# Performance work log

Measured on AMD Instinct MI355X. Metric: run time of the kernel, lower is better.

The kernel has to match this reference:

```python
import jax, jax.numpy as jnp
import numpy as np

B, N, D_U = 32, 4096, 64
D = 128          # mlp_dim == model dim after MLP
H = 2            # n_heads
DH = D // H


def setup_inputs() -> dict:
    key = jax.random.key(0)
    ks = jax.random.split(key, 16)
    sc = lambda fan_in: 1.0 / np.sqrt(fan_in)
    inp = {
        "u": jax.random.normal(ks[0], (B, N, D_U), dtype=jnp.float32),
        "x": jax.random.uniform(ks[1], (B, N, 2), dtype=jnp.float32),
        # MLP params: [D_U -> D -> D], gelu after each hidden layer
        "W1": jax.random.normal(ks[2], (D_U, D), dtype=jnp.float32) * sc(D_U),
        "b1": jnp.zeros((D,), jnp.float32),
        "W2": jax.random.normal(ks[3], (D, D), dtype=jnp.float32) * sc(D),
        "b2": jnp.zeros((D,), jnp.float32),
        # learned pooling query (nn.Embed(1, D))
        "embed": jax.random.normal(ks[4], (1, D), dtype=jnp.float32),
        # multihead linear attention projections
        "Wq": jax.random.normal(ks[5], (D, D), dtype=jnp.float32) * sc(D),
        "bq": jnp.zeros((D,), jnp.float32),
        "Wk": jax.random.normal(ks[6], (D, D), dtype=jnp.float32) * sc(D),
        "bk": jnp.zeros((D,), jnp.float32),
        "Wv": jax.random.normal(ks[7], (D, D), dtype=jnp.float32) * sc(D),
        "bv": jnp.zeros((D,), jnp.float32),
        "Wo": jax.random.normal(ks[8], (D, D), dtype=jnp.float32) * sc(D),
        "bo": jnp.zeros((D,), jnp.float32),
    }
    return inp


def reference(u, x, W1, b1, W2, b2, embed, Wq, bq, Wk, bk, Wv, bv, Wo, bo):
    # MLP on set elements: [B, N, D_U] -> [B, N, D]
    z = jax.nn.gelu(u @ W1 + b1)
    z = jax.nn.gelu(z @ W2 + b2)

    n = z.shape[1]
    # learned query broadcast over batch: [B, 1, D]
    s = jnp.broadcast_to(embed[None, :, :], (z.shape[0], 1, z.shape[-1]))

    # multihead linear (Galerkin-style, softmax-free) attention
    q = (s @ Wq + bq).reshape(z.shape[0], 1, H, DH)   # [B, 1, H, DH]
    k = (z @ Wk + bk).reshape(z.shape[0], n, H, DH)   # [B, N, H, DH]
    v = (z @ Wv + bv).reshape(z.shape[0], n, H, DH)   # [B, N, H, DH]

    # context = K^T V / N per head: [B, H, DH, DH]
    context = jnp.einsum("bnhd,bnhe->bhde", k, v) / n
    out = jnp.einsum("bqhd,bhde->bqhe", q, context)   # [B, 1, H, DH]
    out = out.reshape(z.shape[0], 1, D) @ Wo + bo     # [B, 1, D]

    return out[:, 0, :]                               # [B, D]
```

## Files before the change

### kernel.cpp

```cpp
#include <hip/hip_runtime.h>
#include <math.h>

#define Bsz 32
#define Nn  4096
#define DU  64
#define Dm  128

#define GRID_MLP 512
#define BPB 16

#define WS_WKQ 0
#define WS_BKQ 256
#define WS_CNT 288
#define WS_A   320
#define WS_S   384
#define WS_WP  8576

#define H1STR 136

typedef short frag_ab __attribute__((ext_vector_type(8)));
typedef float frag_cd __attribute__((ext_vector_type(4)));

__device__ __forceinline__ unsigned short f2bf(float x) {
    union { float f; unsigned int u; } c; c.f = x;
    unsigned int r = c.u + 0x7fffu + ((c.u >> 16) & 1u);
    return (unsigned short)(r >> 16);
}

__device__ __forceinline__ float gelu_fast(float x) {
    float t = x * x;
    float a = x * fmaf(t, -0.1029432f, -2.3022081f);
    float e = __builtin_amdgcn_exp2f(a);
    return x * __builtin_amdgcn_rcpf(1.0f + e);
}

__global__ __launch_bounds__(256) void precompute_kernel(
    const float* __restrict__ embed, const float* __restrict__ Wq,
    const float* __restrict__ bq, const float* __restrict__ Wk,
    const float* __restrict__ bk, const float* __restrict__ W1,
    const float* __restrict__ W2, float* __restrict__ ws)
{
    __shared__ float qv[128];
    const int tid = threadIdx.x;
    const int bid = blockIdx.x;

    if (bid < 12) {
        const int e = bid * 256 + tid;
        const int f = e >> 6, L = e & 63;
        const int q2 = L >> 4, n = L & 15;
        const float* src;
        int ks, nt;
        if (f < 16) { src = W1; ks = f >> 3;        nt = f & 7; }
        else        { src = W2; ks = (f - 16) >> 3; nt = (f - 16) & 7; }
        const int kb = ks * 32 + q2 * 8;
        const int c  = nt * 16 + n;
        unsigned int p[4];
        #pragma unroll
        for (int jj = 0; jj < 4; ++jj) {
            unsigned int lo = f2bf(src[(kb + 2 * jj)     * Dm + c]);
            unsigned int hi = f2bf(src[(kb + 2 * jj + 1) * Dm + c]);
            p[jj] = lo | (hi << 16);
        }
        ((uint4*)(ws + WS_WP))[e] = make_uint4(p[0], p[1], p[2], p[3]);
    } else if (bid == 12) {
        if (tid < 128) {
            float s = bq[tid];
            #pragma unroll 8
            for (int j = 0; j < 128; ++j) s += embed[j] * Wq[j * 128 + tid];
            qv[tid] = s;
        }
        __syncthreads();
        if (tid < 128) {
            float s0 = 0.f, s1 = 0.f;
            #pragma unroll 8
            for (int dh = 0; dh < 64; ++dh) {
                s0 += Wk[tid * 128 + dh]      * qv[dh];
                s1 += Wk[tid * 128 + 64 + dh] * qv[64 + dh];
            }
            ws[WS_WKQ + tid]       = s0;
            ws[WS_WKQ + 128 + tid] = s1;
        }
        if (tid < 2) {
            float s = 0.f;
            for (int dh = 0; dh < 64; ++dh) s += bk[tid * 64 + dh] * qv[tid * 64 + dh];
            ws[WS_BKQ + tid] = s;
        }
    } else {
        for (int idx = WS_CNT + tid; idx < WS_WP; idx += 256) ws[idx] = 0.f;
    }
}

__global__ __launch_bounds__(512) void mlp_pool_kernel(
    const float* __restrict__ u,  const float* __restrict__ b1,
    const float* __restrict__ b2, const float* __restrict__ Wv,
    const float* __restrict__ bv, const float* __restrict__ Wo,
    const float* __restrict__ bo, float* __restrict__ ws,
    float* __restrict__ out)
{
    __shared__ short lds_w[48 * 512];
    __shared__ short lds_h1[4 * 16 * H1STR];
    __shared__ float a2buf[4][16][2][2];
    __shared__ int   do_epi;

    const int tid  = threadIdx.x;
    const int wave = tid >> 6;
    const int lane = tid & 63;
    const int quad = lane >> 4;
    const int n15  = lane & 15;
    const int p    = wave >> 1;
    const int hf   = wave & 1;

    {
        const float4* src = (const float4*)(ws + WS_WP);
        float4* dst = (float4*)lds_w;
        #pragma unroll
        for (int i = 0; i < 6; ++i) dst[tid + 512 * i] = src[tid + 512 * i];
    }

    float b1c[4], b2c[4], wkq0[4], wkq1[4];
    #pragma unroll
    for (int nt = 0; nt < 4; ++nt) {
        const int c = hf * 64 + nt * 16 + n15;
        b1c[nt]  = b1[c];
        b2c[nt]  = b2[c];
        wkq0[nt] = ws[WS_WKQ + c];
        wkq1[nt] = ws[WS_WKQ + 128 + c];
    }
    const float bkq0 = ws[WS_BKQ];
    const float bkq1 = ws[WS_BKQ + 1];
    __syncthreads();

    const int bb = blockIdx.x >> 4;
    const int jb = blockIdx.x & 15;
    short* h1t = lds_h1 + p * 16 * H1STR;

    float s0p[4], s1p[4];
    #pragma unroll
    for (int nt = 0; nt < 4; ++nt) { s0p[nt] = 0.f; s1p[nt] = 0.f; }
    float aA0 = 0.f, aA1 = 0.f;

    const float* ub = u + ((size_t)(bb * Nn + jb * 256 + p * 16 + n15)) * DU + quad * 8;
    float4 f0 = *(const float4*)(ub);
    float4 f1 = *(const float4*)(ub + 4);
    float4 f2 = *(const float4*)(ub + 32);
    float4 f3 = *(const float4*)(ub + 36);

    #pragma unroll 1
    for (int it = 0; it < 4; ++it) {
        frag_ab a0, a1;
        a0[0] = (short)f2bf(f0.x); a0[1] = (short)f2bf(f0.y);
        a0[2] = (short)f2bf(f0.z); a0[3] = (short)f2bf(f0.w);
        a0[4] = (short)f2bf(f1.x); a0[5] = (short)f2bf(f1.y);
        a0[6] = (short)f2bf(f1.z); a0[7] = (short)f2bf(f1.w);
        a1[0] = (short)f2bf(f2.x); a1[1] = (short)f2bf(f2.y);
        a1[2] = (short)f2bf(f2.z); a1[3] = (short)f2bf(f2.w);
        a1[4] = (short)f2bf(f3.x); a1[5] = (short)f2bf(f3.y);
        a1[6] = (short)f2bf(f3.z); a1[7] = (short)f2bf(f3.w);

        if (it < 3) {
            const float* un = ub + (size_t)((it + 1) * 64) * DU;
            f0 = *(const float4*)(un);
            f1 = *(const float4*)(un + 4);
            f2 = *(const float4*)(un + 32);
            f3 = *(const float4*)(un + 36);
        }

        frag_cd acc[4];
        #pragma unroll
        for (int nt = 0; nt < 4; ++nt) acc[nt] = (frag_cd){0.f, 0.f, 0.f, 0.f};
        #pragma unroll
        for (int nt = 0; nt < 4; ++nt) {
            const int f = hf * 4 + nt;
            frag_ab w0 = *(const frag_ab*)&lds_w[(f)     * 512 + lane * 8];
            acc[nt] = __builtin_amdgcn_mfma_f32_16x16x32_bf16(a0, w0, acc[nt], 0, 0, 0);
            frag_ab w1 = *(const frag_ab*)&lds_w[(8 + f) * 512 + lane * 8];
            acc[nt] = __builtin_amdgcn_mfma_f32_16x16x32_bf16(a1, w1, acc[nt], 0, 0, 0);
        }

        #pragma unroll
        for (int nt = 0; nt < 4; ++nt) {
            #pragma unroll
            for (int r = 0; r < 4; ++r) {
                float g = gelu_fast(acc[nt][r] + b1c[nt]);
                h1t[(quad * 4 + r) * H1STR + hf * 64 + nt * 16 + n15] = (short)f2bf(g);
            }
        }
        __syncthreads();

        frag_cd acc2[4];
        #pragma unroll
        for (int nt = 0; nt < 4; ++nt) acc2[nt] = (frag_cd){0.f, 0.f, 0.f, 0.f};
        #pragma unroll
        for (int ks = 0; ks < 4; ++ks) {
            frag_ab a2 = *(const frag_ab*)&h1t[n15 * H1STR + ks * 32 + quad * 8];
            #pragma unroll
            for (int nt = 0; nt < 4; ++nt) {
                frag_ab w2f = *(const frag_ab*)&lds_w[(16 + ks * 8 + hf * 4 + nt) * 512 + lane * 8];
                acc2[nt] = __builtin_amdgcn_mfma_f32_16x16x32_bf16(a2, w2f, acc2[nt], 0, 0, 0);
            }
        }

        #pragma unroll
        for (int nt = 0; nt < 4; ++nt) {
            #pragma unroll
            for (int r = 0; r < 4; ++r)
                acc2[nt][r] = gelu_fast(acc2[nt][r] + b2c[nt]);
        }

        float p0[4], p1[4];
        #pragma unroll
        for (int r = 0; r < 4; ++r) { p0[r] = 0.f; p1[r] = 0.f; }
        #pragma unroll
        for (int nt = 0; nt < 4; ++nt) {
            #pragma unroll
            for (int r = 0; r < 4; ++r) {
                p0[r] += acc2[nt][r] * wkq0[nt];
                p1[r] += acc2[nt][r] * wkq1[nt];
            }
        }
        #pragma unroll
        for (int r = 0; r < 4; ++r) {
            #pragma unroll
            for (int d = 1; d < 16; d <<= 1) {
                p0[r] += __shfl_xor(p0[r], d);
                p1[r] += __shfl_xor(p1[r], d);
            }
        }
        if (n15 == 0) {
            #pragma unroll
            for (int r = 0; r < 4; ++r) {
                const int row = quad * 4 + r;
                a2buf[p][row][0][hf] = p0[r];
                a2buf[p][row][1][hf] = p1[r];
            }
        }
        __syncthreads();

        #pragma unroll
        for (int r = 0; r < 4; ++r) {
            const int row = quad * 4 + r;
            const float al0 = a2buf[p][row][0][0] + a2buf[p][row][0][1] + bkq0;
            const float al1 = a2buf[p][row][1][0] + a2buf[p][row][1][1] + bkq1;
            #pragma unroll
            for (int nt = 0; nt < 4; ++nt) {
                s0p[nt] += al0 * acc2[nt][r];
                s1p[nt] += al1 * acc2[nt][r];
            }
            aA0 += al0; aA1 += al1;
        }
    }

    #pragma unroll
    for (int nt = 0; nt < 4; ++nt) {
        s0p[nt] += __shfl_xor(s0p[nt], 16); s0p[nt] += __shfl_xor(s0p[nt], 32);
        s1p[nt] += __shfl_xor(s1p[nt], 16); s1p[nt] += __shfl_xor(s1p[nt], 32);
    }
    aA0 += __shfl_xor(aA0, 16); aA0 += __shfl_xor(aA0, 32);
    aA1 += __shfl_xor(aA1, 16); aA1 += __shfl_xor(aA1, 32);

    if (quad == 0) {
        #pragma unroll
        for (int nt = 0; nt < 4; ++nt) {
            const int c = hf * 64 + nt * 16 + n15;
            atomicAdd(&ws[WS_S + (bb * 2 + 0) * 128 + c], s0p[nt]);
            atomicAdd(&ws[WS_S + (bb * 2 + 1) * 128 + c], s1p[nt]);
        }
    }
    if (hf == 0 && lane == 0) {
        atomicAdd(&ws[WS_A + bb * 2 + 0], aA0);
        atomicAdd(&ws[WS_A + bb * 2 + 1], aA1);
    }

    __syncthreads();
    if (tid == 0) {
        __threadfence();
        int old = atomicAdd((int*)ws + WS_CNT + bb, 1);
        do_epi = (old == BPB - 1) ? 1 : 0;
    }
    __syncthreads();

    if (do_epi) {
        float* eb     = (float*)lds_h1;
        float* e_sS   = eb;
        float* e_sA   = eb + 256;
        float* e_pool = eb + 264;
        float* e_part = eb + 392;

        if (tid < 256) e_sS[tid] = atomicAdd(&ws[WS_S + bb * 256 + tid], 0.f);
        if (tid < 2)   e_sA[tid] = atomicAdd(&ws[WS_A + bb * 2 + tid], 0.f);
        __syncthreads();

        const int i = tid & 127, seg = tid >> 7;
        const int h = i >> 6;
        {
            float dot = 0.f;
            #pragma unroll 8
            for (int d0 = 0; d0 < 32; ++d0) {
                const int d = seg * 32 + d0;
                dot += e_sS[h * 128 + d] * Wv[d * 128 + i];
            }
            e_part[tid] = dot;
        }
        __syncthreads();
        if (tid < 128)
            e_pool[i] = (e_part[i] + e_part[128 + i] + e_part[256 + i] + e_part[384 + i]
                         + e_sA[h] * bv[i]) * (1.0f / 4096.0f);
        __syncthreads();

        {
            float o = 0.f;
            #pragma unroll 8
            for (int d0 = 0; d0 < 32; ++d0) {
                const int d = seg * 32 + d0;
                o += e_pool[d] * Wo[d * 128 + i];
            }
            e_part[tid] = o;
        }
        __syncthreads();
        if (tid < 128)
            out[bb * 128 + i] = bo[i] + e_part[i] + e_part[128 + i] + e_part[256 + i] + e_part[384 + i];
    }
}

extern "C" void kernel_launch(void* const* d_in, const int* in_sizes, int n_in,
                              void* d_out, int out_size, void* d_ws, size_t ws_size,
                              hipStream_t stream) {
    const float* u     = (const float*)d_in[0];
    const float* W1    = (const float*)d_in[2];
    const float* b1    = (const float*)d_in[3];
    const float* W2    = (const float*)d_in[4];
    const float* b2    = (const float*)d_in[5];
    const float* embed = (const float*)d_in[6];
    const float* Wq    = (const float*)d_in[7];
    const float* bq    = (const float*)d_in[8];
    const float* Wk    = (const float*)d_in[9];
    const float* bk    = (const float*)d_in[10];
    const float* Wv    = (const float*)d_in[11];
    const float* bv    = (const float*)d_in[12];
    const float* Wo    = (const float*)d_in[13];
    const float* bo    = (const float*)d_in[14];
    float* ws  = (float*)d_ws;
    float* out = (float*)d_out;

    hipLaunchKernelGGL(precompute_kernel, dim3(14), dim3(256), 0, stream,
                       embed, Wq, bq, Wk, bk, W1, W2, ws);
    hipLaunchKernelGGL(mlp_pool_kernel, dim3(GRID_MLP), dim3(512), 0, stream,
                       u, b1, b2, Wv, bv, Wo, bo, ws, out);
}
```

Before: 150.3 us.

## Make each wave own a full 16-row tile, removing block barriers from MLP loop

Restructures the fused MLP+pooling kernel so each wave computes all 128 output columns for its own 16 rows instead of splitting columns across wave pairs. The per-iteration __syncthreads and LDS exchange of partial key-query dots go away, and the first-layer weights are read straight from global memory (transposed MFMA operand order) instead of being staged in LDS. The completion counter becomes per-wave, so the last wave of a batch runs the epilogue alone. This removes block-wide barriers and LDS traffic, at the cost of more registers per wave, repeated global reads of W1 fragments, and a serial single-wave epilogue.

```diff
diff --git a/kernel.cpp b/kernel.cpp
--- a/kernel.cpp
+++ b/kernel.cpp
@@ -7,7 +7,8 @@
 #define Dm  128
 
 #define GRID_MLP 512
-#define BPB 16
+#define NWAVE 8
+#define WAVES_PER_BATCH 128
 
 #define WS_WKQ 0
 #define WS_BKQ 256
@@ -97,56 +98,55 @@
     const float* __restrict__ bo, float* __restrict__ ws,
     float* __restrict__ out)
 {
-    __shared__ short lds_w[48 * 512];
-    __shared__ short lds_h1[4 * 16 * H1STR];
-    __shared__ float a2buf[4][16][2][2];
-    __shared__ int   do_epi;
+    __shared__ short lds_w2[32 * 512];
+    __shared__ float b1_lds[128];
+    __shared__ short lds_h1[NWAVE * 16 * H1STR];
 
     const int tid  = threadIdx.x;
     const int wave = tid >> 6;
     const int lane = tid & 63;
-    const int quad = lane >> 4;
+    const int q    = lane >> 4;
     const int n15  = lane & 15;
-    const int p    = wave >> 1;
-    const int hf   = wave & 1;
-
-    {
-        const float4* src = (const float4*)(ws + WS_WP);
-        float4* dst = (float4*)lds_w;
-        #pragma unroll
-        for (int i = 0; i < 6; ++i) dst[tid + 512 * i] = src[tid + 512 * i];
-    }
-
-    float b1c[4], b2c[4], wkq0[4], wkq1[4];
-    #pragma unroll
-    for (int nt = 0; nt < 4; ++nt) {
-        const int c = hf * 64 + nt * 16 + n15;
-        b1c[nt]  = b1[c];
-        b2c[nt]  = b2[c];
-        wkq0[nt] = ws[WS_WKQ + c];
-        wkq1[nt] = ws[WS_WKQ + 128 + c];
-    }
-    const float bkq0 = ws[WS_BKQ];
-    const float bkq1 = ws[WS_BKQ + 1];
-    __syncthreads();
-
-    const int bb = blockIdx.x >> 4;
-    const int jb = blockIdx.x & 15;
-    short* h1t = lds_h1 + p * 16 * H1STR;
-
-    float s0p[4], s1p[4];
-    #pragma unroll
-    for (int nt = 0; nt < 4; ++nt) { s0p[nt] = 0.f; s1p[nt] = 0.f; }
-    float aA0 = 0.f, aA1 = 0.f;
-
-    const float* ub = u + ((size_t)(bb * Nn + jb * 256 + p * 16 + n15)) * DU + quad * 8;
+
+    const int g  = blockIdx.x * NWAVE + wave;
+    const int bb = g >> 7;
+    const int jt = g & 127;
+
+    const float* ub = u + ((size_t)(bb * Nn + jt * 16 + n15)) * DU + q * 8;
     float4 f0 = *(const float4*)(ub);
     float4 f1 = *(const float4*)(ub + 4);
     float4 f2 = *(const float4*)(ub + 32);
     float4 f3 = *(const float4*)(ub + 36);
 
+    const uint4* wsrc = (const uint4*)(ws + WS_WP);
+    {
+        uint4* dst = (uint4*)lds_w2;
+        #pragma unroll
+        for (int i = 0; i < 4; ++i) dst[tid + 512 * i] = wsrc[1024 + tid + 512 * i];
+        if (tid < 128) b1_lds[tid] = b1[tid];
+    }
+
+    float wkq0[8], wkq1[8], b2c[8];
+    #pragma unroll
+    for (int ct = 0; ct < 8; ++ct) {
+        const int c = ct * 16 + n15;
+        wkq0[ct] = ws[WS_WKQ + c];
+        wkq1[ct] = ws[WS_WKQ + 128 + c];
+        b2c[ct]  = b2[c];
+    }
+    const float bkq0 = ws[WS_BKQ];
+    const float bkq1 = ws[WS_BKQ + 1];
+    __syncthreads();
+
+    short* h1w = lds_h1 + wave * 16 * H1STR;
+
+    float s0p[8], s1p[8];
+    #pragma unroll
+    for (int ct = 0; ct < 8; ++ct) { s0p[ct] = 0.f; s1p[ct] = 0.f; }
+    float aA0 = 0.f, aA1 = 0.f;
+
     #pragma unroll 1
-    for (int it = 0; it < 4; ++it) {
+    for (int t = 0; t < 2; ++t) {
         frag_ab a0, a1;
         a0[0] = (short)f2bf(f0.x); a0[1] = (short)f2bf(f0.y);
         a0[2] = (short)f2bf(f0.z); a0[3] = (short)f2bf(f0.w);
@@ -157,65 +157,58 @@
         a1[4] = (short)f2bf(f3.x); a1[5] = (short)f2bf(f3.y);
         a1[6] = (short)f2bf(f3.z); a1[7] = (short)f2bf(f3.w);
 
-        if (it < 3) {
-            const float* un = ub + (size_t)((it + 1) * 64) * DU;
+        if (t == 0) {
+            const float* un = ub + (size_t)2048 * DU;
             f0 = *(const float4*)(un);
             f1 = *(const float4*)(un + 4);
             f2 = *(const float4*)(un + 32);
             f3 = *(const float4*)(un + 36);
         }
 
-        frag_cd acc[4];
-        #pragma unroll
-        for (int nt = 0; nt < 4; ++nt) acc[nt] = (frag_cd){0.f, 0.f, 0.f, 0.f};
-        #pragma unroll
-        for (int nt = 0; nt < 4; ++nt) {
-            const int f = hf * 4 + nt;
-            frag_ab w0 = *(const frag_ab*)&lds_w[(f)     * 512 + lane * 8];
-            acc[nt] = __builtin_amdgcn_mfma_f32_16x16x32_bf16(a0, w0, acc[nt], 0, 0, 0);
-            frag_ab w1 = *(const frag_ab*)&lds_w[(8 + f) * 512 + lane * 8];
-            acc[nt] = __builtin_amdgcn_mfma_f32_16x16x32_bf16(a1, w1, acc[nt], 0, 0, 0);
-        }
-
-        #pragma unroll
-        for (int nt = 0; nt < 4; ++nt) {
+        #pragma unroll
+        for (int ct = 0; ct < 8; ++ct) {
+            float4 bi = *(const float4*)&b1_lds[ct * 16 + q * 4];
+            frag_cd acc = (frag_cd){bi.x, bi.y, bi.z, bi.w};
+            frag_ab w0 = *(const frag_ab*)&wsrc[(ct)     * 64 + lane];
+            acc = __builtin_amdgcn_mfma_f32_16x16x32_bf16(w0, a0, acc, 0, 0, 0);
+            frag_ab w1 = *(const frag_ab*)&wsrc[(8 + ct) * 64 + lane];
+            acc = __builtin_amdgcn_mfma_f32_16x16x32_bf16(w1, a1, acc, 0, 0, 0);
+            unsigned int lo = (unsigned int)f2bf(gelu_fast(acc[0]))
+                            | ((unsigned int)f2bf(gelu_fast(acc[1])) << 16);
+            unsigned int hi = (unsigned int)f2bf(gelu_fast(acc[2]))
+                            | ((unsigned int)f2bf(gelu_fast(acc[3])) << 16);
+            *(uint2*)&h1w[n15 * H1STR + ct * 16 + q * 4] = make_uint2(lo, hi);
+        }
+
+        frag_cd acc2[8];
+        #pragma unroll
+        for (int ct = 0; ct < 8; ++ct)
+            acc2[ct] = (frag_cd){b2c[ct], b2c[ct], b2c[ct], b2c[ct]};
+        #pragma unroll
+        for (int ks = 0; ks < 4; ++ks) {
+            frag_ab af = *(const frag_ab*)&h1w[n15 * H1STR + ks * 32 + q * 8];
+            #pragma unroll
+            for (int ct = 0; ct < 8; ++ct) {
+                frag_ab bf = *(const frag_ab*)&lds_w2[(ks * 8 + ct) * 512 + lane * 8];
+                acc2[ct] = __builtin_amdgcn_mfma_f32_16x16x32_bf16(af, bf, acc2[ct], 0, 0, 0);
+            }
+        }
+        #pragma unroll
+        for (int ct = 0; ct < 8; ++ct) {
+            #pragma unroll
+            for (int r = 0; r < 4; ++r)
+                acc2[ct][r] = gelu_fast(acc2[ct][r]);
+        }
+
+        float p0[4], p1[4];
+        #pragma unroll
+        for (int r = 0; r < 4; ++r) { p0[r] = 0.f; p1[r] = 0.f; }
+        #pragma unroll
+        for (int ct = 0; ct < 8; ++ct) {
             #pragma unroll
             for (int r = 0; r < 4; ++r) {
-                float g = gelu_fast(acc[nt][r] + b1c[nt]);
-                h1t[(quad * 4 + r) * H1STR + hf * 64 + nt * 16 + n15] = (short)f2bf(g);
-            }
-        }
-        __syncthreads();
-
-        frag_cd acc2[4];
-        #pragma unroll
-        for (int nt = 0; nt < 4; ++nt) acc2[nt] = (frag_cd){0.f, 0.f, 0.f, 0.f};
-        #pragma unroll
-        for (int ks = 0; ks < 4; ++ks) {
-            frag_ab a2 = *(const frag_ab*)&h1t[n15 * H1STR + ks * 32 + quad * 8];
-            #pragma unroll
-            for (int nt = 0; nt < 4; ++nt) {
-                frag_ab w2f = *(const frag_ab*)&lds_w[(16 + ks * 8 + hf * 4 + nt) * 512 + lane * 8];
-                acc2[nt] = __builtin_amdgcn_mfma_f32_16x16x32_bf16(a2, w2f, acc2[nt], 0, 0, 0);
-            }
-        }
-
-        #pragma unroll
-        for (int nt = 0; nt < 4; ++nt) {
-            #pragma unroll
-            for (int r = 0; r < 4; ++r)
-                acc2[nt][r] = gelu_fast(acc2[nt][r] + b2c[nt]);
-        }
-
-        float p0[4], p1[4];
-        #pragma unroll
-        for (int r = 0; r < 4; ++r) { p0[r] = 0.f; p1[r] = 0.f; }
-        #pragma unroll
-        for (int nt = 0; nt < 4; ++nt) {
-            #pragma unroll
-            for (int r = 0; r < 4; ++r) {
-                p0[r] += acc2[nt][r] * wkq0[nt];
-                p1[r] += acc2[nt][r] * wkq1[nt];
+                p0[r] += acc2[ct][r] * wkq0[ct];
+                p1[r] += acc2[ct][r] * wkq1[ct];
             }
         }
         #pragma unroll
@@ -226,99 +219,72 @@
                 p1[r] += __shfl_xor(p1[r], d);
             }
         }
-        if (n15 == 0) {
-            #pragma unroll
-            for (int r = 0; r < 4; ++r) {
-                const int row = quad * 4 + r;
-                a2buf[p][row][0][hf] = p0[r];
-                a2buf[p][row][1][hf] = p1[r];
-            }
-        }
-        __syncthreads();
-
         #pragma unroll
         for (int r = 0; r < 4; ++r) {
-            const int row = quad * 4 + r;
-            const float al0 = a2buf[p][row][0][0] + a2buf[p][row][0][1] + bkq0;
-            const float al1 = a2buf[p][row][1][0] + a2buf[p][row][1][1] + bkq1;
-            #pragma unroll
-            for (int nt = 0; nt < 4; ++nt) {
-                s0p[nt] += al0 * acc2[nt][r];
-                s1p[nt] += al1 * acc2[nt][r];
+            const float al0 = p0[r] + bkq0;
+            const float al1 = p1[r] + bkq1;
+            #pragma unroll
+            for (int ct = 0; ct < 8; ++ct) {
+                s0p[ct] += al0 * acc2[ct][r];
+                s1p[ct] += al1 * acc2[ct][r];
             }
             aA0 += al0; aA1 += al1;
         }
     }
 
     #pragma unroll
-    for (int nt = 0; nt < 4; ++nt) {
-        s0p[nt] += __shfl_xor(s0p[nt], 16); s0p[nt] += __shfl_xor(s0p[nt], 32);
-        s1p[nt] += __shfl_xor(s1p[nt], 16); s1p[nt] += __shfl_xor(s1p[nt], 32);
+    for (int ct = 0; ct < 8; ++ct) {
+        s0p[ct] += __shfl_xor(s0p[ct], 16); s0p[ct] += __shfl_xor(s0p[ct], 32);
+        s1p[ct] += __shfl_xor(s1p[ct], 16); s1p[ct] += __shfl_xor(s1p[ct], 32);
     }
     aA0 += __shfl_xor(aA0, 16); aA0 += __shfl_xor(aA0, 32);
     aA1 += __shfl_xor(aA1, 16); aA1 += __shfl_xor(aA1, 32);
 
-    if (quad == 0) {
-        #pragma unroll
-        for (int nt = 0; nt < 4; ++nt) {
-            const int c = hf * 64 + nt * 16 + n15;
-            atomicAdd(&ws[WS_S + (bb * 2 + 0) * 128 + c], s0p[nt]);
-            atomicAdd(&ws[WS_S + (bb * 2 + 1) * 128 + c], s1p[nt]);
-        }
-    }
-    if (hf == 0 && lane == 0) {
+    if (q == 0) {
+        #pragma unroll
+        for (int ct = 0; ct < 8; ++ct) {
+            const int c = ct * 16 + n15;
+            atomicAdd(&ws[WS_S + (bb * 2 + 0) * 128 + c], s0p[ct]);
+            atomicAdd(&ws[WS_S + (bb * 2 + 1) * 128 + c], s1p[ct]);
+        }
+    }
+    if (lane == 0) {
         atomicAdd(&ws[WS_A + bb * 2 + 0], aA0);
         atomicAdd(&ws[WS_A + bb * 2 + 1], aA1);
     }
 
-    __syncthreads();
-    if (tid == 0) {
+    __threadfence();
+    int old = 0;
+    if (lane == 0) old = atomicAdd((int*)ws + WS_CNT + bb, 1);
+    old = __shfl(old, 0);
+    if (old == WAVES_PER_BATCH - 1) {
         __threadfence();
-        int old = atomicAdd((int*)ws + WS_CNT + bb, 1);
-        do_epi = (old == BPB - 1) ? 1 : 0;
-    }
-    __syncthreads();
-
-    if (do_epi) {
-        float* eb     = (float*)lds_h1;
-        float* e_sS   = eb;
-        float* e_sA   = eb + 256;
-        float* e_pool = eb + 264;
-        float* e_part = eb + 392;
-
-        if (tid < 256) e_sS[tid] = atomicAdd(&ws[WS_S + bb * 256 + tid], 0.f);
-        if (tid < 2)   e_sA[tid] = atomicAdd(&ws[WS_A + bb * 2 + tid], 0.f);
-        __syncthreads();
-
-        const int i = tid & 127, seg = tid >> 7;
-        const int h = i >> 6;
-        {
-            float dot = 0.f;
-            #pragma unroll 8
-            for (int d0 = 0; d0 < 32; ++d0) {
-                const int d = seg * 32 + d0;
-                dot += e_sS[h * 128 + d] * Wv[d * 128 + i];
-            }
-            e_part[tid] = dot;
-        }
-        __syncthreads();
-        if (tid < 128)
-            e_pool[i] = (e_part[i] + e_part[128 + i] + e_part[256 + i] + e_part[384 + i]
-                         + e_sA[h] * bv[i]) * (1.0f / 4096.0f);
-        __syncthreads();
-
-        {
-            float o = 0.f;
-            #pragma unroll 8
-            for (int d0 = 0; d0 < 32; ++d0) {
-                const int d = seg * 32 + d0;
-                o += e_pool[d] * Wo[d * 128 + i];
-            }
-            e_part[tid] = o;
-        }
-        __syncthreads();
-        if (tid < 128)
-            out[bb * 128 + i] = bo[i] + e_part[i] + e_part[128 + i] + e_part[256 + i] + e_part[384 + i];
+        float* sc = (float*)h1w;
+        #pragma unroll
+        for (int k = 0; k < 4; ++k)
+            sc[lane + 64 * k] = atomicAdd(&ws[WS_S + bb * 256 + lane + 64 * k], 0.f);
+        if (lane < 2) sc[256 + lane] = atomicAdd(&ws[WS_A + bb * 2 + lane], 0.f);
+
+        const int c0 = lane, c1 = lane + 64;
+        const float sa0 = sc[256], sa1 = sc[257];
+        float d0 = sa0 * bv[c0], d1 = sa1 * bv[c1];
+        #pragma unroll 8
+        for (int d = 0; d < 128; ++d) {
+            d0 += sc[d]       * Wv[d * 128 + c0];
+            d1 += sc[128 + d] * Wv[d * 128 + c1];
+        }
+        sc[272 + c0] = d0 * (1.0f / 4096.0f);
+        sc[272 + c1] = d1 * (1.0f / 4096.0f);
+
+        float o0 = bo[c0], o1 = bo[c1];
+        #pragma unroll 8
+        for (int d = 0; d < 128; ++d) {
+            const float pd = sc[272 + d];
+            o0 += pd * Wo[d * 128 + c0];
+            o1 += pd * Wo[d * 128 + c1];
+        }
+        out[bb * 128 + c0] = o0;
+        out[bb * 128 + c1] = o1;
     }
 }
 
```

Measured after the change: 397.5 us. 165% more time.
